# Optimization experiments

Measured on AMD Instinct MI355X. Metric: run time of the kernel, lower is better.

Reference implementation:

```python
import jax, jax.numpy as jnp
import numpy as np

W_BIJ, W_ORTH, W_LAP, W_PRE = 1000.0, 1000.0, 1.0, 100000.0
N, V, C, K = 8, 5000, 128, 128
NUM_DESC = int(C * 0.2)  # 25, matches sub_pre=0.2


def setup_inputs() -> dict:
    key = jax.random.key(0)
    ks = jax.random.split(key, 10)
    return {
        "C12": jax.random.normal(ks[0], (N, K, K), jnp.float32) * 0.1,
        "C21": jax.random.normal(ks[1], (N, K, K), jnp.float32) * 0.1,
        "feat_1": jax.random.normal(ks[2], (N, V, C), jnp.float32),
        "feat_2": jax.random.normal(ks[3], (N, V, C), jnp.float32),
        "evecs_1": jax.random.normal(ks[4], (N, V, K), jnp.float32) * 0.02,
        "evecs_2": jax.random.normal(ks[5], (N, V, K), jnp.float32) * 0.02,
        "evecs_trans1": jax.random.normal(ks[6], (N, K, V), jnp.float32) * 0.02,
        "evecs_trans2": jax.random.normal(ks[7], (N, K, V), jnp.float32) * 0.02,
        "evals_1": jax.random.uniform(ks[8], (N, K), jnp.float32),
        "evals_2": jax.random.uniform(ks[9], (N, K), jnp.float32),
        "desc_ind": jnp.arange(NUM_DESC, dtype=jnp.int32),
    }


def _frob3(a, b):
    # torch FrobeniusLoss on [N,K,K]: mean over batch of sum((a-b)^2, dims (1,2))
    return jnp.mean(jnp.sum((a - b) ** 2, axis=(1, 2)))


def reference(C12, C21, feat_1, feat_2, evecs_1, evecs_2,
              evecs_trans1, evecs_trans2, evals_1, evals_2, desc_ind):
    n, k, _ = C12.shape
    eye = jnp.eye(k, dtype=C12.dtype)[None]  # broadcasts over batch

    l_bij = (_frob3(jnp.einsum('nij,njk->nik', C12, C21), eye)
             + _frob3(jnp.einsum('nij,njk->nik', C21, C12), eye)) * W_BIJ

    l_orth = (_frob3(jnp.einsum('nji,njk->nik', C12, C12), eye)
              + _frob3(jnp.einsum('nji,njk->nik', C21, C21), eye)) * W_ORTH

    # diag-scale commutativity: C * evals (col scale) vs evals * C (row scale)
    l_lap = (_frob3(C12 * evals_1[:, None, :], evals_2[:, :, None] * C12)
             + _frob3(C21 * evals_2[:, None, :], evals_1[:, :, None] * C21)) * W_LAP

    # descriptor preservation via commutativity, D = num_desc subsampled channels
    f1 = feat_1[:, :, desc_ind]  # [N,V,D]
    f2 = feat_2[:, :, desc_ind]
    # M[n,d] = Phi_trans @ diag(f[:,d]) @ Phi  (KxK per descriptor), fused einsum
    M1 = jnp.einsum('nkv,nvd,nvj->ndkj', evecs_trans1, f1, evecs_1)
    M2 = jnp.einsum('nkv,nvd,nvj->ndkj', evecs_trans2, f2, evecs_2)
    s1 = jnp.einsum('nij,ndjk->ndik', C12, M1)  # C12 @ M1_d
    t1 = jnp.einsum('ndij,njk->ndik', M2, C12)  # M2_d @ C12
    s2 = jnp.einsum('nij,ndjk->ndik', C21, M2)
    t2 = jnp.einsum('ndij,njk->ndik', M1, C21)
    # torch FrobeniusLoss on 5D [N,D,1,K,K]: sum over axes (1,2), then global mean
    # over remaining [N,K,K] -> total_sum / (N*K*K)
    denom = jnp.asarray(n * k * k, s1.dtype)
    l_pre = ((jnp.sum((s1 - t1) ** 2) + jnp.sum((s2 - t2) ** 2)) / denom) * W_PRE

    return jnp.stack([l_bij, l_orth, l_lap, l_pre])
```

## Files before the change

### kernel.cpp

```cpp
#include <hip/hip_runtime.h>

typedef float v4f __attribute__((ext_vector_type(4)));
typedef unsigned int u32;
typedef __attribute__((ext_vector_type(4))) u32 u32x4;
typedef __attribute__((ext_vector_type(8))) short bhalf8;

#define K 128
#define W_BIJ 1000.0f
#define W_ORTH 1000.0f
#define W_LAP 1.0f
#define W_PRE 100000.0f

#define NCH 79
#define TILE_B 16384
#define CTILE_B 32768
#define VPAD 5056

union B8 { u32x4 u; bhalf8 h; };

static __device__ __forceinline__ unsigned short f2b(float x) {
    union { float f; unsigned int u; } v; v.f = x;
    unsigned int u = v.u + 0x7FFFu + ((v.u >> 16) & 1u);
    return (unsigned short)(u >> 16);
}
static __device__ __forceinline__ u32 pk2(float lo, float hi) {
    return (u32)f2b(lo) | ((u32)f2b(hi) << 16);
}
static __device__ __forceinline__ float bitsf(u32 x) {
    union { u32 u; float f; } v; v.u = x; return v.f;
}
static __device__ __forceinline__ u32 cvtpk(float lo, float hi) {
    u32 r; asm("v_cvt_pk_bf16_f32 %0, %1, %2" : "=v"(r) : "v"(lo), "v"(hi)); return r;
}
static __device__ __forceinline__ void gload_lds16(const void* g, void* l) {
    __builtin_amdgcn_global_load_lds((const __attribute__((address_space(1))) u32*)g,
                                     (__attribute__((address_space(3))) u32*)l, 16, 0, 0);
}

extern "C" __global__ __launch_bounds__(256, 2)
void surfm_conv(const float* __restrict__ T1, const float* __restrict__ T2,
                const float* __restrict__ E1, const float* __restrict__ E2,
                const float* __restrict__ F1, const float* __restrict__ F2,
                const float* __restrict__ C12g, const float* __restrict__ C21g,
                const int* __restrict__ desc,
                unsigned short* __restrict__ Abf, unsigned short* __restrict__ Ebf,
                float* __restrict__ Fbf, char* __restrict__ Cbf,
                int V, int CF)
{
    __shared__ char csm[32768];
    const int b = blockIdx.x;
    const int tid = threadIdx.x;

    if (b < 1264) {
        const int c  = b % NCH;
        const int mn = b / NCH;
        const float* src = ((mn & 8) ? T2 : T1) + (size_t)(mn & 7) * K * V;
        char* dst = (char*)Abf + (size_t)b * TILE_B;
        #pragma unroll
        for (int it = 0; it < 4; ++it) {
            const int item = it * 256 + tid;
            const int grp = item & 7, r = item >> 3;
            const int kg = grp ^ (r & 7);
            const int k = c * 64 + kg * 8;
            u32x4 o = (u32x4){0u,0u,0u,0u};
            if (k + 8 <= V) {
                const v4f lo = *(const v4f*)(src + (size_t)r * V + k);
                const v4f hi = *(const v4f*)(src + (size_t)r * V + k + 4);
                o[0] = pk2(lo[0], lo[1]); o[1] = pk2(lo[2], lo[3]);
                o[2] = pk2(hi[0], hi[1]); o[3] = pk2(hi[2], hi[3]);
            }
            *(u32x4*)(dst + r * 128 + grp * 16) = o;
        }
    } else if (b < 2528) {
        const int idx = b - 1264;
        const int c  = idx % NCH;
        const int mn = idx / NCH;
        const float* src = ((mn & 8) ? E2 : E1) + (size_t)(mn & 7) * V * K;
        char* dst = (char*)Ebf + (size_t)idx * TILE_B;
        #pragma unroll
        for (int it = 0; it < 8; ++it) {
            const int item = it * 256 + tid;
            const int vp = item >> 5;
            const int j4 = (item & 31) * 4;
            const int v = c * 64 + vp * 2;
            v4f e0 = {0.f,0.f,0.f,0.f}, e1 = e0;
            if (v < V)     e0 = *(const v4f*)(src + (size_t)v * K + j4);
            if (v + 1 < V) e1 = *(const v4f*)(src + (size_t)(v + 1) * K + j4);
            #pragma unroll
            for (int e = 0; e < 4; ++e) {
                const int j = j4 + e;
                *(u32*)(csm + j * 128 + ((vp * 4) ^ ((j & 7) << 4))) = pk2(e0[e], e1[e]);
            }
        }
        __syncthreads();
        #pragma unroll
        for (int it = 0; it < 4; ++it) {
            const int item = it * 256 + tid;
            *(u32x4*)(dst + item * 16) = *(const u32x4*)(csm + item * 16);
        }
    } else if (b < 2928) {
        const int idx = b - 2528;
        const int d  = idx % 25;
        const int mn = idx / 25;
        const int col = desc[d];
        const float* src = ((mn & 8) ? F2 : F1) + (size_t)(mn & 7) * V * CF + col;
        float* dst = Fbf + (size_t)idx * VPAD;
        for (int i = tid; i < VPAD; i += 256)
            dst[i] = (i < V) ? src[(size_t)i * CF] : 0.0f;
    } else {
        const int idx = b - 2928;
        const float* src = ((idx & 8) ? C21g : C12g) + (size_t)(idx & 7) * K * K;
        char* outN = Cbf + (size_t)(idx * 2 + 0) * CTILE_B;
        char* outT = Cbf + (size_t)(idx * 2 + 1) * CTILE_B;
        #pragma unroll
        for (int it = 0; it < 8; ++it) {
            const int item = it * 256 + tid;
            const int r = item >> 4, grp = item & 15;
            const int g = grp ^ (r & 7);
            const v4f lo = *(const v4f*)(src + r * K + g * 8);
            const v4f hi = *(const v4f*)(src + r * K + g * 8 + 4);
            u32x4 o;
            o[0] = pk2(lo[0], lo[1]); o[1] = pk2(lo[2], lo[3]);
            o[2] = pk2(hi[0], hi[1]); o[3] = pk2(hi[2], hi[3]);
            *(u32x4*)(outN + r * 256 + grp * 16) = o;
        }
        #pragma unroll
        for (int it = 0; it < 8; ++it) {
            const int item = it * 256 + tid;
            const int rp = item >> 5;
            const int j4 = (item & 31) * 4;
            const v4f r0 = *(const v4f*)(src + (2 * rp) * K + j4);
            const v4f r1 = *(const v4f*)(src + (2 * rp + 1) * K + j4);
            #pragma unroll
            for (int e = 0; e < 4; ++e) {
                const int j = j4 + e;
                *(u32*)(csm + j * 256 + ((rp * 4) ^ ((j & 7) << 4))) = pk2(r0[e], r1[e]);
            }
        }
        __syncthreads();
        #pragma unroll
        for (int it = 0; it < 8; ++it) {
            const int item = it * 256 + tid;
            *(u32x4*)(outT + item * 16) = *(const u32x4*)(csm + item * 16);
        }
    }
}

extern "C" __global__ __launch_bounds__(512, 2)
void surfm_stage1(const char* __restrict__ Abf, const char* __restrict__ Ebf,
                  const float* __restrict__ Fbf, char* __restrict__ Mbf)
{
    extern __shared__ char sm[];
    const int tid = threadIdx.x;
    const int l  = tid & 63;
    const int wv = tid >> 6;
    const int wq = __builtin_amdgcn_readfirstlane(wv);
    const int b = blockIdx.x;
    const int n = b & 7;
    const int rest = b >> 3;
    const int mat = rest & 1;
    const int dgi = rest >> 1;
    const int d0 = dgi * 2;
    const bool hasD1 = (d0 + 1) < 25;

    const int mn = mat * 8 + n;
    const char* gA = Abf + (size_t)mn * NCH * TILE_B;
    const char* gE = Ebf + (size_t)mn * NCH * TILE_B;
    const char* gW = (const char*)(Fbf + ((size_t)mn * 25 + d0) * VPAD);

    const int stile = wq >> 2;
    const int squad = wq & 3;
    const char* gsrc0 = stile ? gE : gA;
    char* lb0 = sm + stile * 32768;

    const int wm = wq >> 2, wj = wq & 3;
    const int moff = wm * 64, joff = wj * 32;
    const int lm = l & 15;
    const int lk = (l >> 4) * 8;

    v4f acc[2][4][2];
    #pragma unroll
    for (int dd = 0; dd < 2; ++dd)
        #pragma unroll
        for (int mf = 0; mf < 4; ++mf)
            #pragma unroll
            for (int jf = 0; jf < 2; ++jf)
                acc[dd][mf][jf] = (v4f){0.f,0.f,0.f,0.f};

    for (int i = wq; i < 40; i += 8)
        gload_lds16(gW + i * 1024 + l * 16, sm + 65536 + i * 1024);
    {
        const char* gs = gsrc0 + squad * 4096 + l * 16;
        char* ld = lb0 + squad * 4096;
        #pragma unroll
        for (int i = 0; i < 4; ++i)
            gload_lds16(gs + i * 1024, ld + i * 1024);
    }
    asm volatile("s_waitcnt vmcnt(0)" ::: "memory");
    __builtin_amdgcn_s_barrier();

    #pragma unroll 1
    for (int c = 0; c < NCH; ++c) {
        const int par = c & 1;
        if (c + 1 < NCH) {
            const char* gs = gsrc0 + (size_t)(c + 1) * TILE_B + squad * 4096 + l * 16;
            char* ld = lb0 + (par ^ 1) * 16384 + squad * 4096;
            #pragma unroll
            for (int i = 0; i < 4; ++i)
                gload_lds16(gs + i * 1024, ld + i * 1024);
            asm volatile("s_waitcnt vmcnt(4)" ::: "memory");
        } else {
            asm volatile("s_waitcnt vmcnt(0)" ::: "memory");
        }
        __builtin_amdgcn_s_barrier();
        __builtin_amdgcn_sched_barrier(0);

        const char* Ab = sm + par * 16384;
        const char* Eb = sm + 32768 + par * 16384;
        #pragma unroll
        for (int ks = 0; ks < 2; ++ks) {
            const int kb = ks * 64 + lk * 2;
            const float* pw0 = (const float*)(sm + 65536 + c * 256 + ks * 128) + lk;
            const float* pw1 = (const float*)(sm + 65536 + 20224 + c * 256 + ks * 128) + lk;
            const v4f w0a = *(const v4f*)pw0, w0b = *(const v4f*)(pw0 + 4);
            const v4f w1a = *(const v4f*)pw1, w1b = *(const v4f*)(pw1 + 4);
            const float wl0[4] = {w0a[0], w0a[2], w0b[0], w0b[2]};
            const float wh0[4] = {w0a[1], w0a[3], w0b[1], w0b[3]};
            const float wl1[4] = {w1a[0], w1a[2], w1b[0], w1b[2]};
            const float wh1[4] = {w1a[1], w1a[3], w1b[1], w1b[3]};
            B8 p0[2], p1[2];
            #pragma unroll
            for (int jf = 0; jf < 2; ++jf) {
                const int j = joff + jf * 16 + lm;
                const u32x4 e = *(const u32x4*)(Eb + j * 128 + (kb ^ ((j & 7) << 4)));
                #pragma unroll
                for (int t = 0; t < 4; ++t) {
                    const float elo = bitsf(e[t] << 16);
                    const float ehi = bitsf(e[t] & 0xFFFF0000u);
                    p0[jf].u[t] = cvtpk(elo * wl0[t], ehi * wh0[t]);
                    p1[jf].u[t] = cvtpk(elo * wl1[t], ehi * wh1[t]);
                }
            }
            #pragma unroll
            for (int mf = 0; mf < 4; ++mf) {
                const int r = moff + mf * 16 + lm;
                B8 a; a.u = *(const u32x4*)(Ab + r * 128 + (kb ^ ((r & 7) << 4)));
                #pragma unroll
                for (int jf = 0; jf < 2; ++jf) {
                    acc[0][mf][jf] = __builtin_amdgcn_mfma_f32_16x16x32_bf16(a.h, p0[jf].h, acc[0][mf][jf], 0, 0, 0);
                    acc[1][mf][jf] = __builtin_amdgcn_mfma_f32_16x16x32_bf16(a.h, p1[jf].h, acc[1][mf][jf], 0, 0, 0);
                }
            }
        }
        __builtin_amdgcn_s_barrier();
    }

    float* ML = (float*)sm;
    #pragma unroll 1
    for (int dd = 0; dd < 2; ++dd) {
        if (dd == 1 && !hasD1) break;
        __syncthreads();
        #pragma unroll
        for (int mf = 0; mf < 4; ++mf)
            #pragma unroll
            for (int jf = 0; jf < 2; ++jf)
                #pragma unroll
                for (int rg = 0; rg < 4; ++rg) {
                    const int row = moff + mf * 16 + (l >> 4) * 4 + rg;
                    const int col = joff + jf * 16 + lm;
                    ML[row * 132 + col] = acc[dd][mf][jf][rg];
                }
        __syncthreads();
        const int dcur = d0 + dd;
        char* outN = Mbf + (size_t)((n * 25 + dcur) * 2 + mat) * 65536;
        char* outT = outN + 32768;
        #pragma unroll
        for (int it = 0; it < 8; ++it) {
            const int item = it * 512 + tid;
            const int lay = item >> 11;
            const int g2 = item & 2047;
            const int r = g2 >> 4, grp = g2 & 15;
            const int g = grp ^ (r & 7);
            u32x4 o;
            if (lay == 0) {
                const float* p = ML + r * 132 + g * 8;
                const v4f a = *(const v4f*)p, bq = *(const v4f*)(p + 4);
                o[0] = pk2(a[0], a[1]);  o[1] = pk2(a[2], a[3]);
                o[2] = pk2(bq[0], bq[1]); o[3] = pk2(bq[2], bq[3]);
                *(u32x4*)(outN + r * 256 + grp * 16) = o;
            } else {
                const float* p = ML + (g * 8) * 132 + r;
                o[0] = pk2(p[0],   p[132]); o[1] = pk2(p[264], p[396]);
                o[2] = pk2(p[528], p[660]); o[3] = pk2(p[792], p[924]);
                *(u32x4*)(outT + r * 256 + grp * 16) = o;
            }
        }
    }
}

extern "C" __global__ __launch_bounds__(256, 1)
void surfm_stage2(const float* __restrict__ C12g, const float* __restrict__ C21g,
                  const float* __restrict__ ev1g, const float* __restrict__ ev2g,
                  const char* __restrict__ Cbf, const char* __restrict__ Mbf,
                  float* __restrict__ out, int N, int ND)
{
    extern __shared__ char sm[];
    const int b = blockIdx.x;
    const int tid = threadIdx.x;
    const int nPre = N * ND;

    if (b < nPre) {
        const int n = b & 7, d = b >> 3;
        const size_t slot = n * 25 + d;
        const int l = tid & 63;
        const int wq = __builtin_amdgcn_readfirstlane(tid >> 6);
        const int lm = l & 15, lk = (l >> 4) * 8;
        const int wm = wq >> 1, wj = wq & 1;
        float rsum = 0.0f;

        #pragma unroll 1
        for (int ph = 0; ph < 2; ++ph) {
            const char* s0 = Cbf + ((size_t)(ph * 8 + n) * 2 + 0) * CTILE_B;
            const char* s1 = Mbf + (slot * 2 + (ph ? 1 : 0)) * 65536 + 32768;
            const char* s2 = Mbf + (slot * 2 + (ph ? 0 : 1)) * 65536;
            const char* s3 = Cbf + ((size_t)(ph * 8 + n) * 2 + 1) * CTILE_B;
            const char* gs = (wq == 0) ? s0 : (wq == 1) ? s1 : (wq == 2) ? s2 : s3;
            char* ld = sm + wq * 32768;
            if (ph) __builtin_amdgcn_s_barrier();
            #pragma unroll
            for (int i = 0; i < 32; ++i)
                gload_lds16(gs + i * 1024 + l * 16, ld + i * 1024);
            asm volatile("s_waitcnt vmcnt(0)" ::: "memory");
            __builtin_amdgcn_s_barrier();
            __builtin_amdgcn_sched_barrier(0);

            v4f as_[4][4], at_[4][4];
            #pragma unroll
            for (int mf = 0; mf < 4; ++mf)
                #pragma unroll
                for (int jf = 0; jf < 4; ++jf) {
                    as_[mf][jf] = (v4f){0.f,0.f,0.f,0.f};
                    at_[mf][jf] = (v4f){0.f,0.f,0.f,0.f};
                }
            #pragma unroll
            for (int ks = 0; ks < 4; ++ks) {
                const int kb = ks * 64 + lk * 2;
                B8 bS[4], bT[4];
                #pragma unroll
                for (int jf = 0; jf < 4; ++jf) {
                    const int j = wj * 64 + jf * 16 + lm;
                    const int off = j * 256 + (kb ^ ((j & 7) << 4));
                    bS[jf].u = *(const u32x4*)(sm + 32768 + off);
                    bT[jf].u = *(const u32x4*)(sm + 98304 + off);
                }
                #pragma unroll
                for (int mf = 0; mf < 4; ++mf) {
                    const int r = wm * 64 + mf * 16 + lm;
                    const int off = r * 256 + (kb ^ ((r & 7) << 4));
                    B8 aS; aS.u = *(const u32x4*)(sm + off);
                    B8 aT; aT.u = *(const u32x4*)(sm + 65536 + off);
                    #pragma unroll
                    for (int jf = 0; jf < 4; ++jf) {
                        as_[mf][jf] = __builtin_amdgcn_mfma_f32_16x16x32_bf16(aS.h, bS[jf].h, as_[mf][jf], 0, 0, 0);
                        at_[mf][jf] = __builtin_amdgcn_mfma_f32_16x16x32_bf16(aT.h, bT[jf].h, at_[mf][jf], 0, 0, 0);
                    }
                }
            }
            #pragma unroll
            for (int mf = 0; mf < 4; ++mf)
                #pragma unroll
                for (int jf = 0; jf < 4; ++jf) {
                    const v4f df = as_[mf][jf] - at_[mf][jf];
                    rsum += df[0]*df[0] + df[1]*df[1] + df[2]*df[2] + df[3]*df[3];
                }
        }
        #pragma unroll
        for (int off = 32; off; off >>= 1) rsum += __shfl_down(rsum, off, 64);
        if (l == 0)
            atomicAdd(out + 3, rsum * (W_PRE / (float)(N * K * K)));
    } else {
        float* lds = (float*)sm;
        const int idx = b - nPre;
        const int n = idx >> 2, p = idx & 3;
        const float* c12 = C12g + (size_t)n * K * K;
        const float* c21 = C21g + (size_t)n * K * K;
        const float* Xg = (p == 1 || p == 3) ? c21 : c12;
        const float* Yg = (p == 0) ? c21 : c12;
        const float* ea = (p == 0) ? ev1g + n * K : ev2g + n * K;
        const float* eb = (p == 0) ? ev2g + n * K : ev1g + n * K;
        float* X = lds;
        float* Y = lds + K * 129;
        const int tx = tid & 15, ty = tid >> 4;
        float lap = 0.0f;
        for (int i = tid; i < K * K / 4; i += 256) {
            const int r = i >> 5, c4 = (i & 31) * 4;
            const v4f x = *(const v4f*)(Xg + r * K + c4);
            X[r * 129 + c4 + 0] = x[0]; X[r * 129 + c4 + 1] = x[1];
            X[r * 129 + c4 + 2] = x[2]; X[r * 129 + c4 + 3] = x[3];
            if (p < 2) {
                const v4f y = *(const v4f*)(Yg + r * K + c4);
                Y[r * 129 + c4 + 0] = y[0]; Y[r * 129 + c4 + 1] = y[1];
                Y[r * 129 + c4 + 2] = y[2]; Y[r * 129 + c4 + 3] = y[3];
                const float ebi = eb[r];
                #pragma unroll
                for (int e = 0; e < 4; ++e) {
                    const float dlt = ea[c4 + e] - ebi;
                    lap += x[e] * x[e] * dlt * dlt;
                }
            }
        }
        __syncthreads();
        const int i0 = ty * 8, k0 = tx * 8;
        float z[8][8];
        #pragma unroll
        for (int i = 0; i < 8; ++i)
            #pragma unroll
            for (int t = 0; t < 8; ++t) z[i][t] = 0.0f;
        for (int j = 0; j < K; ++j) {
            float xi[8], yk[8];
            if (p < 2) {
                #pragma unroll
                for (int i = 0; i < 8; ++i) xi[i] = X[(i0 + i) * 129 + j];
                #pragma unroll
                for (int t = 0; t < 8; ++t) yk[t] = Y[j * 129 + k0 + t];
            } else {
                #pragma unroll
                for (int i = 0; i < 8; ++i) xi[i] = X[j * 129 + i0 + i];
                #pragma unroll
                for (int t = 0; t < 8; ++t) yk[t] = X[j * 129 + k0 + t];
            }
            #pragma unroll
            for (int i = 0; i < 8; ++i)
                #pragma unroll
                for (int t = 0; t < 8; ++t) z[i][t] += xi[i] * yk[t];
        }
        float sacc = 0.0f;
        #pragma unroll
        for (int i = 0; i < 8; ++i)
            #pragma unroll
            for (int t = 0; t < 8; ++t) {
                const float e = z[i][t] - ((i0 + i) == (k0 + t) ? 1.0f : 0.0f);
                sacc += e * e;
            }
        #pragma unroll
        for (int off = 32; off; off >>= 1) {
            sacc += __shfl_down(sacc, off, 64);
            lap  += __shfl_down(lap, off, 64);
        }
        if ((tid & 63) == 0) {
            if (p < 2) {
                atomicAdd(out + 0, sacc * (W_BIJ / (float)N));
                atomicAdd(out + 2, lap * (W_LAP / (float)N));
            } else {
                atomicAdd(out + 1, sacc * (W_ORTH / (float)N));
            }
        }
    }
}

extern "C" __global__ __launch_bounds__(256, 1)
void surfm_fused(const float* __restrict__ C12g, const float* __restrict__ C21g,
                 const float* __restrict__ F1, const float* __restrict__ F2,
                 const float* __restrict__ E1g, const float* __restrict__ E2g,
                 const float* __restrict__ T1, const float* __restrict__ T2,
                 const float* __restrict__ ev1g, const float* __restrict__ ev2g,
                 const int* __restrict__ desc, float* __restrict__ out,
                 int N, int ND, int V, int CF)
{
    extern __shared__ char smem[];
    const int b   = blockIdx.x;
    const int tid = threadIdx.x;
    const int nPre = N * ND;

    if (b < nPre) {
        const int n = b & 7;
        const int d = b >> 3;
        const int col = desc[d];
        const float* A1g = T1 + (size_t)n * K * V;
        const float* A2g = T2 + (size_t)n * K * V;
        const float* B1g = E1g + (size_t)n * V * K;
        const float* B2g = E2g + (size_t)n * V * K;
        const float* w1g = F1 + (size_t)n * V * CF;
        const float* w2g = F2 + (size_t)n * V * CF;

        char* As1 = smem;
        char* As2 = smem + 32768;
        char* Bt1 = smem + 65536;
        char* Bt2 = smem + 98304;

        const int l  = tid & 63;
        const int w  = tid >> 6;
        const int lm = l & 15;
        const int lk = (l >> 4) * 8;

        v4f acc1[8][2], acc2[8][2];
        #pragma unroll
        for (int mf = 0; mf < 8; ++mf)
            #pragma unroll
            for (int jf = 0; jf < 2; ++jf) {
                acc1[mf][jf] = (v4f){0.f,0.f,0.f,0.f};
                acc2[mf][jf] = (v4f){0.f,0.f,0.f,0.f};
            }

        for (int v0 = 0; v0 < V; v0 += 128) {
            __syncthreads();
            #pragma unroll 4
            for (int it = 0; it < 16; ++it) {
                const int i  = it * 256 + tid;
                const int r  = i >> 5;
                const int c4 = (i & 31) * 4;
                const int vg = v0 + c4;
                v4f a1 = {0.f,0.f,0.f,0.f}, a2 = {0.f,0.f,0.f,0.f};
                if (vg < V) {
                    a1 = *(const v4f*)(A1g + (size_t)r * V + vg);
                    a2 = *(const v4f*)(A2g + (size_t)r * V + vg);
                }
                const int byte = (r * 256 + c4 * 2) ^ ((r & 7) << 4);
                short4 p1, p2;
                p1.x = (short)f2b(a1[0]); p1.y = (short)f2b(a1[1]);
                p1.z = (short)f2b(a1[2]); p1.w = (short)f2b(a1[3]);
                p2.x = (short)f2b(a2[0]); p2.y = (short)f2b(a2[1]);
                p2.z = (short)f2b(a2[2]); p2.w = (short)f2b(a2[3]);
                *(short4*)(As1 + byte) = p1;
                *(short4*)(As2 + byte) = p2;
            }
            #pragma unroll 2
            for (int it = 0; it < 8; ++it) {
                const int i  = it * 256 + tid;
                const int j4 = (i & 31) * 4;
                const int vp = (i >> 5) * 2;
                const int va = v0 + vp, vb = va + 1;
                v4f e1a = {0.f,0.f,0.f,0.f}, e1b = e1a, e2a = e1a, e2b = e1a;
                if (va < V) {
                    const float w1 = w1g[(size_t)va * CF + col];
                    const float w2 = w2g[(size_t)va * CF + col];
                    e1a = *(const v4f*)(B1g + (size_t)va * K + j4) * w1;
                    e2a = *(const v4f*)(B2g + (size_t)va * K + j4) * w2;
                }
                if (vb < V) {
                    const float w1 = w1g[(size_t)vb * CF + col];
                    const float w2 = w2g[(size_t)vb * CF + col];
                    e1b = *(const v4f*)(B1g + (size_t)vb * K + j4) * w1;
                    e2b = *(const v4f*)(B2g + (size_t)vb * K + j4) * w2;
                }
                #pragma unroll
                for (int e = 0; e < 4; ++e) {
                    const int j = j4 + e;
                    const int key = (((j & 7) ^ ((j >> 3) & 7)) << 4);
                    const int byte = (j * 256 + vp * 2) ^ key;
                    *(u32*)(Bt1 + byte) = pk2(e1a[e], e1b[e]);
                    *(u32*)(Bt2 + byte) = pk2(e2a[e], e2b[e]);
                }
            }
            __syncthreads();
            #pragma unroll
            for (int ks = 0; ks < 4; ++ks) {
                const int k0 = ks * 32 + lk;
                bhalf8 bB1[2], bB2[2];
                #pragma unroll
                for (int jf = 0; jf < 2; ++jf) {
                    const int j = w * 32 + jf * 16 + lm;
                    const int key = (((j & 7) ^ ((j >> 3) & 7)) << 4);
                    const int byte = (j * 256 + k0 * 2) ^ key;
                    bB1[jf] = *(const bhalf8*)(Bt1 + byte);
                    bB2[jf] = *(const bhalf8*)(Bt2 + byte);
                }
                #pragma unroll
                for (int mf = 0; mf < 8; ++mf) {
                    const int r = mf * 16 + lm;
                    const int byte = (r * 256 + k0 * 2) ^ ((r & 7) << 4);
                    const bhalf8 a1 = *(const bhalf8*)(As1 + byte);
                    const bhalf8 a2 = *(const bhalf8*)(As2 + byte);
                    acc1[mf][0] = __builtin_amdgcn_mfma_f32_16x16x32_bf16(a1, bB1[0], acc1[mf][0], 0, 0, 0);
                    acc1[mf][1] = __builtin_amdgcn_mfma_f32_16x16x32_bf16(a1, bB1[1], acc1[mf][1], 0, 0, 0);
                    acc2[mf][0] = __builtin_amdgcn_mfma_f32_16x16x32_bf16(a2, bB2[0], acc2[mf][0], 0, 0, 0);
                    acc2[mf][1] = __builtin_amdgcn_mfma_f32_16x16x32_bf16(a2, bB2[1], acc2[mf][1], 0, 0, 0);
                }
            }
        }
        __syncthreads();
        float* M1 = (float*)smem;
        float* M2 = (float*)smem + K * K;
        #pragma unroll
        for (int mf = 0; mf < 8; ++mf)
            #pragma unroll
            for (int jf = 0; jf < 2; ++jf)
                #pragma unroll
                for (int rg = 0; rg < 4; ++rg) {
                    const int row = mf * 16 + ((l >> 4) << 2) + rg;
                    const int cj  = w * 32 + jf * 16 + lm;
                    const int pc  = ((((cj >> 2) ^ ((row >> 3) & 7)) << 2) | (cj & 3));
                    M1[row * K + pc] = acc1[mf][jf][rg];
                    M2[row * K + pc] = acc2[mf][jf][rg];
                }
        __syncthreads();

        const int tx = tid & 15, ty = tid >> 4;
        const int r0 = ty * 8;
        const int ca = tx * 4, cb = 64 + tx * 4;
        const int kcol = ty & 7;
        const float* c12 = C12g + (size_t)n * K * K;
        const float* c21 = C21g + (size_t)n * K * K;
        v4f acc1a[8], acc1b[8], acc2a[8], acc2b[8];
        #pragma unroll
        for (int i = 0; i < 8; ++i) {
            acc1a[i] = (v4f){0,0,0,0}; acc1b[i] = (v4f){0,0,0,0};
            acc2a[i] = (v4f){0,0,0,0}; acc2b[i] = (v4f){0,0,0,0};
        }
        for (int j = 0; j < K; ++j) {
            const int keyj = (j >> 3) & 7;
            const int ga = (tx ^ keyj) << 2;
            const int gb = ((16 + tx) ^ keyj) << 2;
            const v4f m1ra = *(const v4f*)(M1 + j * K + ga);
            const v4f m1rb = *(const v4f*)(M1 + j * K + gb);
            const v4f m2ra = *(const v4f*)(M2 + j * K + ga);
            const v4f m2rb = *(const v4f*)(M2 + j * K + gb);
            const v4f c12ra = *(const v4f*)(c12 + j * K + ca);
            const v4f c12rb = *(const v4f*)(c12 + j * K + cb);
            const v4f c21ra = *(const v4f*)(c21 + j * K + ca);
            const v4f c21rb = *(const v4f*)(c21 + j * K + cb);
            const int jp = (((j >> 2) ^ kcol) << 2) | (j & 3);
            #pragma unroll
            for (int i = 0; i < 8; ++i) {
                const int r = r0 + i;
                const float x12 = c12[r * K + j];
                const float x21 = c21[r * K + j];
                const float m1c = M1[r * K + jp];
                const float m2c = M2[r * K + jp];
                acc1a[i] += m1ra * x12; acc1a[i] -= c12ra * m2c;
                acc1b[i] += m1rb * x12; acc1b[i] -= c12rb * m2c;
                acc2a[i] += m2ra * x21; acc2a[i] -= c21ra * m1c;
                acc2b[i] += m2rb * x21; acc2b[i] -= c21rb * m1c;
            }
        }
        float s = 0.0f;
        #pragma unroll
        for (int i = 0; i < 8; ++i)
            #pragma unroll
            for (int e = 0; e < 4; ++e) {
                s += acc1a[i][e] * acc1a[i][e] + acc1b[i][e] * acc1b[i][e];
                s += acc2a[i][e] * acc2a[i][e] + acc2b[i][e] * acc2b[i][e];
            }
        #pragma unroll
        for (int off = 32; off; off >>= 1) s += __shfl_down(s, off, 64);
        if ((tid & 63) == 0)
            atomicAdd(out + 3, s * (W_PRE / (float)(N * K * K)));
    } else {
        float* ldsf = (float*)smem;
        const int idx = b - nPre;
        const int n = idx >> 2, p = idx & 3;
        const float* c12 = C12g + (size_t)n * K * K;
        const float* c21 = C21g + (size_t)n * K * K;
        const float* Xg = (p == 1 || p == 3) ? c21 : c12;
        const float* Yg = (p == 0) ? c21 : c12;
        const float* ea = (p == 0) ? ev1g + n * K : ev2g + n * K;
        const float* eb = (p == 0) ? ev2g + n * K : ev1g + n * K;
        float* X = ldsf;
        float* Y = ldsf + K * 129;
        const int tx = tid & 15, ty = tid >> 4;
        float lap = 0.0f;
        for (int i = tid; i < K * K / 4; i += 256) {
            const int r = i >> 5, c4 = (i & 31) * 4;
            const v4f x = *(const v4f*)(Xg + r * K + c4);
            X[r * 129 + c4 + 0] = x[0]; X[r * 129 + c4 + 1] = x[1];
            X[r * 129 + c4 + 2] = x[2]; X[r * 129 + c4 + 3] = x[3];
            if (p < 2) {
                const v4f y = *(const v4f*)(Yg + r * K + c4);
                Y[r * 129 + c4 + 0] = y[0]; Y[r * 129 + c4 + 1] = y[1];
                Y[r * 129 + c4 + 2] = y[2]; Y[r * 129 + c4 + 3] = y[3];
                const float ebi = eb[r];
                #pragma unroll
                for (int e = 0; e < 4; ++e) {
                    const float dlt = ea[c4 + e] - ebi;
                    lap += x[e] * x[e] * dlt * dlt;
                }
            }
        }
        __syncthreads();
        const int i0 = ty * 8, k0 = tx * 8;
        float z[8][8];
        #pragma unroll
        for (int i = 0; i < 8; ++i)
            #pragma unroll
            for (int t = 0; t < 8; ++t) z[i][t] = 0.0f;
        for (int j = 0; j < K; ++j) {
            float xi[8], yk[8];
            if (p < 2) {
                #pragma unroll
                for (int i = 0; i < 8; ++i) xi[i] = X[(i0 + i) * 129 + j];
                #pragma unroll
                for (int t = 0; t < 8; ++t) yk[t] = Y[j * 129 + k0 + t];
            } else {
                #pragma unroll
                for (int i = 0; i < 8; ++i) xi[i] = X[j * 129 + i0 + i];
                #pragma unroll
                for (int t = 0; t < 8; ++t) yk[t] = X[j * 129 + k0 + t];
            }
            #pragma unroll
            for (int i = 0; i < 8; ++i)
                #pragma unroll
                for (int t = 0; t < 8; ++t) z[i][t] += xi[i] * yk[t];
        }
        float s = 0.0f;
        #pragma unroll
        for (int i = 0; i < 8; ++i)
            #pragma unroll
            for (int t = 0; t < 8; ++t) {
                const float e = z[i][t] - ((i0 + i) == (k0 + t) ? 1.0f : 0.0f);
                s += e * e;
            }
        #pragma unroll
        for (int off = 32; off; off >>= 1) {
            s   += __shfl_down(s, off, 64);
            lap += __shfl_down(lap, off, 64);
        }
        if ((tid & 63) == 0) {
            if (p < 2) {
                atomicAdd(out + 0, s * (W_BIJ / (float)N));
                atomicAdd(out + 2, lap * (W_LAP / (float)N));
            } else {
                atomicAdd(out + 1, s * (W_ORTH / (float)N));
            }
        }
    }
}

extern "C" void kernel_launch(void* const* d_in, const int* in_sizes, int n_in,
                              void* d_out, int out_size, void* d_ws, size_t ws_size,
                              hipStream_t stream) {
    (void)n_in;
    const float* C12 = (const float*)d_in[0];
    const float* C21 = (const float*)d_in[1];
    const float* F1  = (const float*)d_in[2];
    const float* F2  = (const float*)d_in[3];
    const float* E1  = (const float*)d_in[4];
    const float* E2  = (const float*)d_in[5];
    const float* T1  = (const float*)d_in[6];
    const float* T2  = (const float*)d_in[7];
    const float* ev1 = (const float*)d_in[8];
    const float* ev2 = (const float*)d_in[9];
    const int* desc  = (const int*)d_in[10];
    float* out = (float*)d_out;

    const int N  = in_sizes[8] / K;
    const int ND = in_sizes[10];
    const int V  = in_sizes[4] / (N * K);
    const int CF = in_sizes[2] / (N * V);

    hipMemsetAsync(d_out, 0, (size_t)out_size * sizeof(float), stream);

    const size_t ABF = (size_t)16 * NCH * TILE_B;
    const size_t EBF = ABF;
    const size_t FBF = (size_t)400 * VPAD * 4;
    const size_t CBF = (size_t)32 * CTILE_B;
    const size_t MBF = (size_t)400 * 65536;
    const size_t need = ABF + EBF + FBF + CBF + MBF;

    const bool okShape = (N == 8 && ND == 25 && V == 5000 && CF == 128);
    if (!okShape || ws_size < need) {
        const size_t shmem = (size_t)(2 * K * 129) * sizeof(float);
        hipFuncSetAttribute((const void*)surfm_fused,
                            hipFuncAttributeMaxDynamicSharedMemorySize, (int)shmem);
        const int blocks = N * ND + 4 * N;
        surfm_fused<<<blocks, 256, shmem, stream>>>(C12, C21, F1, F2, E1, E2, T1, T2,
                                                    ev1, ev2, desc, out, N, ND, V, CF);
        return;
    }

    char* ws = (char*)d_ws;
    unsigned short* Abf = (unsigned short*)ws;
    unsigned short* Ebf = (unsigned short*)(ws + ABF);
    float* Fbf = (float*)(ws + ABF + EBF);
    char* Cbf = ws + ABF + EBF + FBF;
    char* Mbf = ws + ABF + EBF + FBF + CBF;

    surfm_conv<<<2944, 256, 0, stream>>>(T1, T2, E1, E2, F1, F2, C12, C21, desc,
                                         Abf, Ebf, Fbf, Cbf, V, CF);

    const size_t shmem1 = 106496;
    hipFuncSetAttribute((const void*)surfm_stage1,
                        hipFuncAttributeMaxDynamicSharedMemorySize, (int)shmem1);
    surfm_stage1<<<208, 512, shmem1, stream>>>((const char*)Abf, (const char*)Ebf,
                                               Fbf, Mbf);

    const size_t shmem2 = 132096;
    hipFuncSetAttribute((const void*)surfm_stage2,
                        hipFuncAttributeMaxDynamicSharedMemorySize, (int)shmem2);
    surfm_stage2<<<N * ND + 4 * N, 256, shmem2, stream>>>(C12, C21, ev1, ev2,
                                                          Cbf, Mbf, out, N, ND);
}
```

Before: 201.4 us.

## Split stage1 V-reduction across two blocks with fp32 partials and reduce kernel

Stage1 now splits the V-chunk loop into two halves per output slot, doubling the grid to 416 blocks. Each block writes fp32 partial M tiles, either to separate buffers or by atomic adds. A new surfm_mconv kernel sums the partials and emits the bf16 normal and transposed layouts. Each wave now loads its E rows directly from global into registers instead of staging them in LDS. This halves shared memory and raises occupancy, at the cost of an extra kernel launch and fp32 partial traffic.

```diff
diff --git a/kernel.cpp b/kernel.cpp
--- a/kernel.cpp
+++ b/kernel.cpp
@@ -14,7 +14,7 @@
 #define NCH 79
 #define TILE_B 16384
 #define CTILE_B 32768
-#define VPAD 5056
+#define VPAD 5120
 
 union B8 { u32x4 u; bhalf8 h; };
 
@@ -89,7 +89,7 @@
             #pragma unroll
             for (int e = 0; e < 4; ++e) {
                 const int j = j4 + e;
-                *(u32*)(csm + j * 128 + ((vp * 4) ^ ((j & 7) << 4))) = pk2(e0[e], e1[e]);
+                *(u32*)(csm + j * 128 + vp * 4) = pk2(e0[e], e1[e]);
             }
         }
         __syncthreads();
@@ -146,9 +146,10 @@
     }
 }
 
-extern "C" __global__ __launch_bounds__(512, 2)
+extern "C" __global__ __launch_bounds__(512, 4)
 void surfm_stage1(const char* __restrict__ Abf, const char* __restrict__ Ebf,
-                  const float* __restrict__ Fbf, char* __restrict__ Mbf)
+                  const float* __restrict__ Fbf, float* __restrict__ Mpart,
+                  int partStride)
 {
     extern __shared__ char sm[];
     const int tid = threadIdx.x;
@@ -157,7 +158,8 @@
     const int wq = __builtin_amdgcn_readfirstlane(wv);
     const int b = blockIdx.x;
     const int n = b & 7;
-    const int rest = b >> 3;
+    const int vh = (b >> 3) & 1;
+    const int rest = b >> 4;
     const int mat = rest & 1;
     const int dgi = rest >> 1;
     const int d0 = dgi * 2;
@@ -166,48 +168,51 @@
     const int mn = mat * 8 + n;
     const char* gA = Abf + (size_t)mn * NCH * TILE_B;
     const char* gE = Ebf + (size_t)mn * NCH * TILE_B;
-    const char* gW = (const char*)(Fbf + ((size_t)mn * 25 + d0) * VPAD);
-
-    const int stile = wq >> 2;
-    const int squad = wq & 3;
-    const char* gsrc0 = stile ? gE : gA;
-    char* lb0 = sm + stile * 32768;
-
-    const int wm = wq >> 2, wj = wq & 3;
-    const int moff = wm * 64, joff = wj * 32;
+    const char* gW = (const char*)(Fbf + ((size_t)mn * 25 + d0) * VPAD) + vh * 10240;
+
+    const int c0 = vh ? 40 : 0;
+    const int NT = vh ? 39 : 40;
+
     const int lm = l & 15;
     const int lk = (l >> 4) * 8;
-
-    v4f acc[2][4][2];
+    const int j  = wq * 16 + lm;
+    const int rkey = (lm & 7) << 4;
+    float* wLds = (float*)(sm + 32768);
+
+    v4f acc0[8], acc1[8];
     #pragma unroll
-    for (int dd = 0; dd < 2; ++dd)
-        #pragma unroll
-        for (int mf = 0; mf < 4; ++mf)
-            #pragma unroll
-            for (int jf = 0; jf < 2; ++jf)
-                acc[dd][mf][jf] = (v4f){0.f,0.f,0.f,0.f};
-
-    for (int i = wq; i < 40; i += 8)
-        gload_lds16(gW + i * 1024 + l * 16, sm + 65536 + i * 1024);
+    for (int mf = 0; mf < 8; ++mf) {
+        acc0[mf] = (v4f){0.f,0.f,0.f,0.f};
+        acc1[mf] = (v4f){0.f,0.f,0.f,0.f};
+    }
+
+    for (int i = wq; i < 20; i += 8) {
+        const int dd = i / 10, off = (i - dd * 10) * 1024;
+        gload_lds16(gW + dd * 20480 + off + l * 16, sm + 32768 + dd * 10240 + off);
+    }
     {
-        const char* gs = gsrc0 + squad * 4096 + l * 16;
-        char* ld = lb0 + squad * 4096;
-        #pragma unroll
-        for (int i = 0; i < 4; ++i)
-            gload_lds16(gs + i * 1024, ld + i * 1024);
-    }
+        const char* t = gA + (size_t)c0 * TILE_B;
+        gload_lds16(t + (wq * 2 + 0) * 1024 + l * 16, sm + (wq * 2 + 0) * 1024);
+        gload_lds16(t + (wq * 2 + 1) * 1024 + l * 16, sm + (wq * 2 + 1) * 1024);
+    }
+    const char* gEl = gE + j * 128 + lk * 2;
+    u32x4 eC0 = *(const u32x4*)(gEl + (size_t)c0 * TILE_B);
+    u32x4 eC1 = *(const u32x4*)(gEl + (size_t)c0 * TILE_B + 64);
     asm volatile("s_waitcnt vmcnt(0)" ::: "memory");
     __builtin_amdgcn_s_barrier();
 
     #pragma unroll 1
-    for (int c = 0; c < NCH; ++c) {
-        const int par = c & 1;
-        if (c + 1 < NCH) {
-            const char* gs = gsrc0 + (size_t)(c + 1) * TILE_B + squad * 4096 + l * 16;
-            char* ld = lb0 + (par ^ 1) * 16384 + squad * 4096;
-            #pragma unroll
-            for (int i = 0; i < 4; ++i)
-                gload_lds16(gs + i * 1024, ld + i * 1024);
+    for (int t = 0; t < NT; ++t) {
+        const int par = t & 1;
+        u32x4 eN0 = eC0, eN1 = eC1;
+        if (t + 1 < NT) {
+            const char* tA = gA + (size_t)(c0 + t + 1) * TILE_B;
+            char* dA = sm + (par ^ 1) * 16384;
+            gload_lds16(tA + (wq * 2 + 0) * 1024 + l * 16, dA + (wq * 2 + 0) * 1024);
+            gload_lds16(tA + (wq * 2 + 1) * 1024 + l * 16, dA + (wq * 2 + 1) * 1024);
+            const char* tE = gEl + (size_t)(c0 + t + 1) * TILE_B;
+            eN0 = *(const u32x4*)(tE);
+            eN1 = *(const u32x4*)(tE + 64);
             asm volatile("s_waitcnt vmcnt(4)" ::: "memory");
         } else {
             asm volatile("s_waitcnt vmcnt(0)" ::: "memory");
@@ -216,84 +221,103 @@
         __builtin_amdgcn_sched_barrier(0);
 
         const char* Ab = sm + par * 16384;
-        const char* Eb = sm + 32768 + par * 16384;
         #pragma unroll
         for (int ks = 0; ks < 2; ++ks) {
-            const int kb = ks * 64 + lk * 2;
-            const float* pw0 = (const float*)(sm + 65536 + c * 256 + ks * 128) + lk;
-            const float* pw1 = (const float*)(sm + 65536 + 20224 + c * 256 + ks * 128) + lk;
+            const u32x4 e = ks ? eC1 : eC0;
+            const float* pw0 = wLds + t * 64 + ks * 32 + lk;
+            const float* pw1 = pw0 + 2560;
             const v4f w0a = *(const v4f*)pw0, w0b = *(const v4f*)(pw0 + 4);
             const v4f w1a = *(const v4f*)pw1, w1b = *(const v4f*)(pw1 + 4);
             const float wl0[4] = {w0a[0], w0a[2], w0b[0], w0b[2]};
             const float wh0[4] = {w0a[1], w0a[3], w0b[1], w0b[3]};
             const float wl1[4] = {w1a[0], w1a[2], w1b[0], w1b[2]};
             const float wh1[4] = {w1a[1], w1a[3], w1b[1], w1b[3]};
-            B8 p0[2], p1[2];
-            #pragma unroll
-            for (int jf = 0; jf < 2; ++jf) {
-                const int j = joff + jf * 16 + lm;
-                const u32x4 e = *(const u32x4*)(Eb + j * 128 + (kb ^ ((j & 7) << 4)));
-                #pragma unroll
-                for (int t = 0; t < 4; ++t) {
-                    const float elo = bitsf(e[t] << 16);
-                    const float ehi = bitsf(e[t] & 0xFFFF0000u);
-                    p0[jf].u[t] = cvtpk(elo * wl0[t], ehi * wh0[t]);
-                    p1[jf].u[t] = cvtpk(elo * wl1[t], ehi * wh1[t]);
-                }
-            }
-            #pragma unroll
-            for (int mf = 0; mf < 4; ++mf) {
-                const int r = moff + mf * 16 + lm;
-                B8 a; a.u = *(const u32x4*)(Ab + r * 128 + (kb ^ ((r & 7) << 4)));
-                #pragma unroll
-                for (int jf = 0; jf < 2; ++jf) {
-                    acc[0][mf][jf] = __builtin_amdgcn_mfma_f32_16x16x32_bf16(a.h, p0[jf].h, acc[0][mf][jf], 0, 0, 0);
-                    acc[1][mf][jf] = __builtin_amdgcn_mfma_f32_16x16x32_bf16(a.h, p1[jf].h, acc[1][mf][jf], 0, 0, 0);
-                }
-            }
-        }
+            B8 p0, p1;
+            #pragma unroll
+            for (int t4 = 0; t4 < 4; ++t4) {
+                const float elo = bitsf(e[t4] << 16);
+                const float ehi = bitsf(e[t4] & 0xFFFF0000u);
+                p0.u[t4] = cvtpk(elo * wl0[t4], ehi * wh0[t4]);
+                p1.u[t4] = cvtpk(elo * wl1[t4], ehi * wh1[t4]);
+            }
+            const int kb = ks * 64 + lk * 2;
+            #pragma unroll
+            for (int mf = 0; mf < 8; ++mf) {
+                const int r = mf * 16 + lm;
+                B8 a; a.u = *(const u32x4*)(Ab + r * 128 + (kb ^ rkey));
+                acc0[mf] = __builtin_amdgcn_mfma_f32_16x16x32_bf16(a.h, p0.h, acc0[mf], 0, 0, 0);
+                acc1[mf] = __builtin_amdgcn_mfma_f32_16x16x32_bf16(a.h, p1.h, acc1[mf], 0, 0, 0);
+            }
+        }
+        eC0 = eN0; eC1 = eN1;
         __builtin_amdgcn_s_barrier();
     }
 
-    float* ML = (float*)sm;
-    #pragma unroll 1
-    for (int dd = 0; dd < 2; ++dd) {
-        if (dd == 1 && !hasD1) break;
-        __syncthreads();
-        #pragma unroll
-        for (int mf = 0; mf < 4; ++mf)
-            #pragma unroll
-            for (int jf = 0; jf < 2; ++jf)
-                #pragma unroll
-                for (int rg = 0; rg < 4; ++rg) {
-                    const int row = moff + mf * 16 + (l >> 4) * 4 + rg;
-                    const int col = joff + jf * 16 + lm;
-                    ML[row * 132 + col] = acc[dd][mf][jf][rg];
-                }
-        __syncthreads();
-        const int dcur = d0 + dd;
-        char* outN = Mbf + (size_t)((n * 25 + dcur) * 2 + mat) * 65536;
-        char* outT = outN + 32768;
-        #pragma unroll
-        for (int it = 0; it < 8; ++it) {
-            const int item = it * 512 + tid;
-            const int lay = item >> 11;
-            const int g2 = item & 2047;
-            const int r = g2 >> 4, grp = g2 & 15;
-            const int g = grp ^ (r & 7);
-            u32x4 o;
-            if (lay == 0) {
-                const float* p = ML + r * 132 + g * 8;
-                const v4f a = *(const v4f*)p, bq = *(const v4f*)(p + 4);
-                o[0] = pk2(a[0], a[1]);  o[1] = pk2(a[2], a[3]);
-                o[2] = pk2(bq[0], bq[1]); o[3] = pk2(bq[2], bq[3]);
-                *(u32x4*)(outN + r * 256 + grp * 16) = o;
-            } else {
-                const float* p = ML + (g * 8) * 132 + r;
-                o[0] = pk2(p[0],   p[132]); o[1] = pk2(p[264], p[396]);
-                o[2] = pk2(p[528], p[660]); o[3] = pk2(p[792], p[924]);
-                *(u32x4*)(outT + r * 256 + grp * 16) = o;
-            }
+    const int slotM = (n * 25 + d0) * 2 + mat;
+    const int rbase = (l >> 4) * 4;
+    {
+        float* dst = Mpart + ((size_t)(vh * partStride + slotM)) * 16384 + j * 128 + rbase;
+        if (partStride) {
+            #pragma unroll
+            for (int mf = 0; mf < 8; ++mf) *(v4f*)(dst + mf * 16) = acc0[mf];
+        } else {
+            #pragma unroll
+            for (int mf = 0; mf < 8; ++mf)
+                #pragma unroll
+                for (int e = 0; e < 4; ++e) atomicAdd(dst + mf * 16 + e, acc0[mf][e]);
+        }
+    }
+    if (hasD1) {
+        float* dst = Mpart + ((size_t)(vh * partStride + slotM + 2)) * 16384 + j * 128 + rbase;
+        if (partStride) {
+            #pragma unroll
+            for (int mf = 0; mf < 8; ++mf) *(v4f*)(dst + mf * 16) = acc1[mf];
+        } else {
+            #pragma unroll
+            for (int mf = 0; mf < 8; ++mf)
+                #pragma unroll
+                for (int e = 0; e < 4; ++e) atomicAdd(dst + mf * 16 + e, acc1[mf][e]);
+        }
+    }
+}
+
+extern "C" __global__ __launch_bounds__(256, 2)
+void surfm_mconv(const float* __restrict__ Mpart, int nPart,
+                 char* __restrict__ Mbf)
+{
+    extern __shared__ char sm[];
+    float* sMT = (float*)sm;
+    const int s = blockIdx.x;
+    const int tid = threadIdx.x;
+    const float* p0 = Mpart + (size_t)s * 16384;
+    for (int i = tid; i < 4096; i += 256) {
+        const int jj = i >> 5, r4 = (i & 31) * 4;
+        v4f v = *(const v4f*)(p0 + jj * 128 + r4);
+        if (nPart == 2) v += *(const v4f*)(p0 + (size_t)400 * 16384 + jj * 128 + r4);
+        *(v4f*)(sMT + jj * 132 + r4) = v;
+    }
+    __syncthreads();
+    char* outN = Mbf + (size_t)s * 65536;
+    char* outT = outN + 32768;
+    #pragma unroll
+    for (int it = 0; it < 16; ++it) {
+        const int item = it * 256 + tid;
+        const int lay = item >> 11;
+        const int g2 = item & 2047;
+        const int rr = g2 >> 4, grp = g2 & 15;
+        const int g = grp ^ (rr & 7);
+        u32x4 o;
+        if (lay == 0) {
+            const float* p = sMT + rr * 132 + g * 8;
+            const v4f a = *(const v4f*)p, bq = *(const v4f*)(p + 4);
+            o[0] = pk2(a[0], a[1]);   o[1] = pk2(a[2], a[3]);
+            o[2] = pk2(bq[0], bq[1]); o[3] = pk2(bq[2], bq[3]);
+            *(u32x4*)(outT + rr * 256 + grp * 16) = o;
+        } else {
+            const float* p = sMT + (g * 8) * 132 + rr;
+            o[0] = pk2(p[0],   p[132]); o[1] = pk2(p[264], p[396]);
+            o[2] = pk2(p[528], p[660]); o[3] = pk2(p[792], p[924]);
+            *(u32x4*)(outN + rr * 256 + grp * 16) = o;
         }
     }
 }
@@ -348,8 +372,8 @@
                 B8 bS[4], bT[4];
                 #pragma unroll
                 for (int jf = 0; jf < 4; ++jf) {
-                    const int j = wj * 64 + jf * 16 + lm;
-                    const int off = j * 256 + (kb ^ ((j & 7) << 4));
+                    const int jj = wj * 64 + jf * 16 + lm;
+                    const int off = jj * 256 + (kb ^ ((jj & 7) << 4));
                     bS[jf].u = *(const u32x4*)(sm + 32768 + off);
                     bT[jf].u = *(const u32x4*)(sm + 98304 + off);
                 }
@@ -416,18 +440,18 @@
         for (int i = 0; i < 8; ++i)
             #pragma unroll
             for (int t = 0; t < 8; ++t) z[i][t] = 0.0f;
-        for (int j = 0; j < K; ++j) {
+        for (int jj = 0; jj < K; ++jj) {
             float xi[8], yk[8];
             if (p < 2) {
                 #pragma unroll
-                for (int i = 0; i < 8; ++i) xi[i] = X[(i0 + i) * 129 + j];
-                #pragma unroll
-                for (int t = 0; t < 8; ++t) yk[t] = Y[j * 129 + k0 + t];
+                for (int i = 0; i < 8; ++i) xi[i] = X[(i0 + i) * 129 + jj];
+                #pragma unroll
+                for (int t = 0; t < 8; ++t) yk[t] = Y[jj * 129 + k0 + t];
             } else {
                 #pragma unroll
-                for (int i = 0; i < 8; ++i) xi[i] = X[j * 129 + i0 + i];
-                #pragma unroll
-                for (int t = 0; t < 8; ++t) yk[t] = X[j * 129 + k0 + t];
+                for (int i = 0; i < 8; ++i) xi[i] = X[jj * 129 + i0 + i];
+                #pragma unroll
+                for (int t = 0; t < 8; ++t) yk[t] = X[jj * 129 + k0 + t];
             }
             #pragma unroll
             for (int i = 0; i < 8; ++i)
@@ -607,24 +631,24 @@
             acc1a[i] = (v4f){0,0,0,0}; acc1b[i] = (v4f){0,0,0,0};
             acc2a[i] = (v4f){0,0,0,0}; acc2b[i] = (v4f){0,0,0,0};
         }
-        for (int j = 0; j < K; ++j) {
-            const int keyj = (j >> 3) & 7;
+        for (int jj = 0; jj < K; ++jj) {
+            const int keyj = (jj >> 3) & 7;
             const int ga = (tx ^ keyj) << 2;
             const int gb = ((16 + tx) ^ keyj) << 2;
-            const v4f m1ra = *(const v4f*)(M1 + j * K + ga);
-            const v4f m1rb = *(const v4f*)(M1 + j * K + gb);
-            const v4f m2ra = *(const v4f*)(M2 + j * K + ga);
-            const v4f m2rb = *(const v4f*)(M2 + j * K + gb);
-            const v4f c12ra = *(const v4f*)(c12 + j * K + ca);
-            const v4f c12rb = *(const v4f*)(c12 + j * K + cb);
-            const v4f c21ra = *(const v4f*)(c21 + j * K + ca);
-            const v4f c21rb = *(const v4f*)(c21 + j * K + cb);
-            const int jp = (((j >> 2) ^ kcol) << 2) | (j & 3);
+            const v4f m1ra = *(const v4f*)(M1 + jj * K + ga);
+            const v4f m1rb = *(const v4f*)(M1 + jj * K + gb);
+            const v4f m2ra = *(const v4f*)(M2 + jj * K + ga);
+            const v4f m2rb = *(const v4f*)(M2 + jj * K + gb);
+            const v4f c12ra = *(const v4f*)(c12 + jj * K + ca);
+            const v4f c12rb = *(const v4f*)(c12 + jj * K + cb);
+            const v4f c21ra = *(const v4f*)(c21 + jj * K + ca);
+            const v4f c21rb = *(const v4f*)(c21 + jj * K + cb);
+            const int jp = (((jj >> 2) ^ kcol) << 2) | (jj & 3);
             #pragma unroll
             for (int i = 0; i < 8; ++i) {
                 const int r = r0 + i;
-                const float x12 = c12[r * K + j];
-                const float x21 = c21[r * K + j];
+                const float x12 = c12[r * K + jj];
+                const float x21 = c21[r * K + jj];
                 const float m1c = M1[r * K + jp];
                 const float m2c = M2[r * K + jp];
                 acc1a[i] += m1ra * x12; acc1a[i] -= c12ra * m2c;
@@ -683,18 +707,18 @@
         for (int i = 0; i < 8; ++i)
             #pragma unroll
             for (int t = 0; t < 8; ++t) z[i][t] = 0.0f;
-        for (int j = 0; j < K; ++j) {
+        for (int jj = 0; jj < K; ++jj) {
             float xi[8], yk[8];
             if (p < 2) {
                 #pragma unroll
-                for (int i = 0; i < 8; ++i) xi[i] = X[(i0 + i) * 129 + j];
-                #pragma unroll
-                for (int t = 0; t < 8; ++t) yk[t] = Y[j * 129 + k0 + t];
+                for (int i = 0; i < 8; ++i) xi[i] = X[(i0 + i) * 129 + jj];
+                #pragma unroll
+                for (int t = 0; t < 8; ++t) yk[t] = Y[jj * 129 + k0 + t];
             } else {
                 #pragma unroll
-                for (int i = 0; i < 8; ++i) xi[i] = X[j * 129 + i0 + i];
-                #pragma unroll
-                for (int t = 0; t < 8; ++t) yk[t] = X[j * 129 + k0 + t];
+                for (int i = 0; i < 8; ++i) xi[i] = X[jj * 129 + i0 + i];
+                #pragma unroll
+                for (int t = 0; t < 8; ++t) yk[t] = X[jj * 129 + k0 + t];
             }
             #pragma unroll
             for (int i = 0; i < 8; ++i)
@@ -754,10 +778,17 @@
     const size_t FBF = (size_t)400 * VPAD * 4;
     const size_t CBF = (size_t)32 * CTILE_B;
     const size_t MBF = (size_t)400 * 65536;
-    const size_t need = ABF + EBF + FBF + CBF + MBF;
+    const size_t MP1 = (size_t)400 * 65536;
+    const size_t base = ABF + EBF + FBF + CBF + MBF;
+    const size_t needPart   = base + 2 * MP1;
+    const size_t needAtomic = base + 1 * MP1;
 
     const bool okShape = (N == 8 && ND == 25 && V == 5000 && CF == 128);
-    if (!okShape || ws_size < need) {
+    int mode = 0;
+    if (okShape && ws_size >= needPart) mode = 2;
+    else if (okShape && ws_size >= needAtomic) mode = 1;
+
+    if (mode == 0) {
         const size_t shmem = (size_t)(2 * K * 129) * sizeof(float);
         hipFuncSetAttribute((const void*)surfm_fused,
                             hipFuncAttributeMaxDynamicSharedMemorySize, (int)shmem);
@@ -773,15 +804,24 @@
     float* Fbf = (float*)(ws + ABF + EBF);
     char* Cbf = ws + ABF + EBF + FBF;
     char* Mbf = ws + ABF + EBF + FBF + CBF;
+    float* Mpart = (float*)(ws + base);
 
     surfm_conv<<<2944, 256, 0, stream>>>(T1, T2, E1, E2, F1, F2, C12, C21, desc,
                                          Abf, Ebf, Fbf, Cbf, V, CF);
 
-    const size_t shmem1 = 106496;
+    if (mode == 1)
+        hipMemsetAsync(Mpart, 0, MP1, stream);
+
+    const size_t shmem1 = 53248;
     hipFuncSetAttribute((const void*)surfm_stage1,
                         hipFuncAttributeMaxDynamicSharedMemorySize, (int)shmem1);
-    surfm_stage1<<<208, 512, shmem1, stream>>>((const char*)Abf, (const char*)Ebf,
-                                               Fbf, Mbf);
+    surfm_stage1<<<416, 512, shmem1, stream>>>((const char*)Abf, (const char*)Ebf,
+                                               Fbf, Mpart, (mode == 2) ? 400 : 0);
+
+    const size_t shmemM = (size_t)128 * 132 * 4;
+    hipFuncSetAttribute((const void*)surfm_mconv,
+                        hipFuncAttributeMaxDynamicSharedMemorySize, (int)shmemM);
+    surfm_mconv<<<400, 256, shmemM, stream>>>(Mpart, (mode == 2) ? 2 : 1, Mbf);
 
     const size_t shmem2 = 132096;
     hipFuncSetAttribute((const void*)surfm_stage2,
```

After: 187.6 us. -6.9%, faster.
